# Kernel optimization log

Measured on AMD Instinct MI355X. Metric: run time of the kernel, lower is better.

Reference implementation:

```python
import jax, jax.numpy as jnp
import numpy as np

B, S, H = 2, 1024, 768
D, HID = 24, 96            # hdim_proj_dim, hdim_mlp_hidden
OUT_HID = 2 * max(128, H // 2)  # val_mlp hidden = 768
VAL_IN = 3 * H             # concat_hadam


def setup_inputs() -> dict:
    key = jax.random.key(0)
    ks = jax.random.split(key, 12)
    def w(k, shape, scale=0.02):
        return jax.random.normal(k, shape, dtype=jnp.float32) * scale
    return {
        "H_j": jax.random.normal(ks[0], (B, S, H), dtype=jnp.float32),
        "H_i": jax.random.normal(ks[1], (B, S, H), dtype=jnp.float32),
        "attn_mask": jnp.ones((B, S), dtype=jnp.float32),
        # p_j / p_i: Linear(H, D, bias=False), torch weight layout [D, H]
        "W_pj": w(ks[2], (D, H)),
        "W_pi": w(ks[3], (D, H)),
        # score_mlp: Linear(4D, HID) -> ReLU -> Linear(HID, 1)
        "W_s1": w(ks[4], (HID, 4 * D)),
        "b_s1": jnp.zeros((HID,), dtype=jnp.float32),
        "W_s2": w(ks[5], (1, HID)),
        "b_s2": jnp.zeros((1,), dtype=jnp.float32),
        # val_mlp: Linear(3H, OUT_HID) -> ReLU -> Linear(OUT_HID, H)
        "W_v1": w(ks[6], (OUT_HID, VAL_IN)),
        "b_v1": jnp.zeros((OUT_HID,), dtype=jnp.float32),
        "W_v2": w(ks[7], (H, OUT_HID)),
        "b_v2": jnp.zeros((H,), dtype=jnp.float32),
        "alpha": jnp.float32(0.05),  # init_gate_hdim
    }


def reference(H_j, H_i, attn_mask, W_pj, W_pi, W_s1, b_s1, W_s2, b_s2,
              W_v1, b_v1, W_v2, b_v2, alpha):
    # low-dim projections: [B,S,D]
    Zj = jnp.einsum('bsh,dh->bsd', H_j, W_pj)
    Zi = jnp.einsum('bsh,dh->bsd', H_i, W_pi)
    b, s, d = Zj.shape
    Zj_p = jnp.broadcast_to(Zj[:, :, None, :], (b, s, s, d))  # row = j (query)
    Zi_p = jnp.broadcast_to(Zi[:, None, :, :], (b, s, s, d))  # col = i (key)
    # 4-term pair features: [B,S,S,4D]
    pair = jnp.concatenate([Zj_p, Zi_p, Zj_p * Zi_p, jnp.abs(Zj_p - Zi_p)], axis=-1)
    # per-pair MLP -> scalar logit
    h = jax.nn.relu(jnp.einsum('bjif,hf->bjih', pair, W_s1) + b_s1)
    logits = jnp.einsum('bjih,oh->bjio', h, W_s2)[..., 0] + b_s2[0]  # [B,S,S]
    # additive key mask (mask over last dim = H_i positions)
    neg = jnp.finfo(logits.dtype).min
    logits = logits + (1.0 - attn_mask[:, None, :]) * neg
    # token_temp == 1.0 -> no temperature scaling
    probs = jax.nn.softmax(logits, axis=-1)
    ctx = jnp.einsum('bji,bih->bjh', probs, H_i)  # [B,S,H]
    # concat_hadam value features
    msg_in = jnp.concatenate([ctx, H_j, ctx * H_j], axis=-1)  # [B,S,3H]
    msg = jax.nn.relu(jnp.einsum('bsf,of->bso', msg_in, W_v1) + b_v1)
    msg = jnp.einsum('bso,ho->bsh', msg, W_v2) + b_v2
    # dropout is identity at inference; hdim_val_residual=False
    return alpha * msg
```

## Files before the change

### kernel.cpp

```cpp
#include <hip/hip_runtime.h>
#include <hip/hip_bf16.h>
#include <math.h>

#define B_ 2
#define S_ 1024
#define H_ 768
#define D_ 24
#define HID_ 96
#define OH_ 768
#define VI_ 2304

typedef short bf16x8 __attribute__((ext_vector_type(8)));
typedef float f32x4 __attribute__((ext_vector_type(4)));
typedef unsigned short u16;

static __device__ __forceinline__ float relu_(float x) { return x > 0.f ? x : 0.f; }

static __device__ __forceinline__ short f2bf(float f) {
    __hip_bfloat16 h = __float2bfloat16(f);
    return *reinterpret_cast<short*>(&h);
}
static __device__ __forceinline__ float bf2f(short s) {
    unsigned u = ((unsigned)(u16)s) << 16;
    return __uint_as_float(u);
}

static __device__ __forceinline__ void gl_lds16(const void* g, void* l) {
    __builtin_amdgcn_global_load_lds(
        (const __attribute__((address_space(1))) unsigned int*)g,
        (__attribute__((address_space(3))) unsigned int*)l, 16, 0, 0);
}

#define NEGF (-3.402823466e38f)

__global__ __launch_bounds__(256) void proj_kernel(
    const float* __restrict__ Hj, const float* __restrict__ Hi,
    const float* __restrict__ Wpj, const float* __restrict__ Wpi,
    float* __restrict__ Zj, float* __restrict__ Zi)
{
    __shared__ float rowj[H_], rowi[H_];
    const int t = blockIdx.x;
    const int tid = threadIdx.x;
    const float* hj = Hj + (size_t)t * H_;
    const float* hi = Hi + (size_t)t * H_;
    for (int x = tid; x < H_; x += 256) { rowj[x] = hj[x]; rowi[x] = hi[x]; }
    __syncthreads();

    const int g = tid & 7;
    for (int o = tid >> 3; o < 2 * D_; o += 32) {
        const float* row;
        const float* w;
        if (o < D_) { row = rowj; w = Wpj + o * H_; }
        else        { row = rowi; w = Wpi + (o - D_) * H_; }
        float s = 0.f;
        #pragma unroll 8
        for (int c = 0; c < H_ / 8; ++c) s += row[g + 8 * c] * w[g + 8 * c];
        s += __shfl_down(s, 4, 8);
        s += __shfl_down(s, 2, 8);
        s += __shfl_down(s, 1, 8);
        if (g == 0) {
            if (o < D_) Zj[(size_t)t * D_ + o] = s;
            else        Zi[(size_t)t * D_ + (o - D_)] = s;
        }
    }
}

__global__ __launch_bounds__(256) void pair_mfma_kernel(
    const float* __restrict__ Zj, const float* __restrict__ Zi,
    const float* __restrict__ Ws1, const float* __restrict__ Ws2,
    const float* __restrict__ bs1, const float* __restrict__ bs2,
    float* __restrict__ P)
{
    __shared__ float sZj32[16][28];
    __shared__ float sZi32[64][28];
    __shared__ short sZj16[16][24];
    __shared__ short sZi16[64][24];

    const int j0 = blockIdx.x * 16, i0 = blockIdx.y * 64, b = blockIdx.z;
    const int tid = threadIdx.x;
    const int lane = tid & 63, wv = tid >> 6;
    const int q = lane & 15, g = lane >> 4;

    for (int x = tid; x < 16 * D_; x += 256) {
        int r = x / D_, c = x % D_;
        float v = Zj[((size_t)(b * S_ + j0 + r)) * D_ + c];
        sZj32[r][c] = v; sZj16[r][c] = f2bf(v);
    }
    for (int x = tid; x < 64 * D_; x += 256) {
        int r = x / D_, c = x % D_;
        float v = Zi[((size_t)(b * S_ + i0 + r)) * D_ + c];
        sZi32[r][c] = v; sZi16[r][c] = f2bf(v);
    }

    bf16x8 wf[6][3];
    #pragma unroll
    for (int nt = 0; nt < 6; ++nt)
        #pragma unroll
        for (int ks = 0; ks < 3; ++ks) {
            const float* wp = Ws1 + (size_t)(nt * 16 + q) * 96 + ks * 32 + g * 8;
            bf16x8 t8;
            #pragma unroll
            for (int e = 0; e < 8; ++e) t8[e] = f2bf(wp[e]);
            wf[nt][ks] = t8;
        }
    float bias_r[6], w2_r[6];
    #pragma unroll
    for (int nt = 0; nt < 6; ++nt) {
        bias_r[nt] = bs1[nt * 16 + q];
        w2_r[nt]   = Ws2[nt * 16 + q];
    }
    const float b2 = bs2[0];
    __syncthreads();

    for (int m = 0; m < 16; ++m) {
        const int t = wv * 16 + m;
        const int jj = t >> 2, iibase = (t & 3) * 16;
        const int ii = iibase + q;

        bf16x8 af[3];
        #pragma unroll
        for (int ks = 0; ks < 3; ++ks) {
            const int c = ks * 4 + g;
            bf16x8 t8;
            if (c < 3) {
                t8 = *(const bf16x8*)&sZj16[jj][c * 8];
            } else if (c < 6) {
                t8 = *(const bf16x8*)&sZi16[ii][(c - 3) * 8];
            } else if (c < 9) {
                const float* zja = &sZj32[jj][(c - 6) * 8];
                const float* zia = &sZi32[ii][(c - 6) * 8];
                #pragma unroll
                for (int e = 0; e < 8; ++e) t8[e] = f2bf(zja[e] * zia[e]);
            } else {
                const float* zja = &sZj32[jj][(c - 9) * 8];
                const float* zia = &sZi32[ii][(c - 9) * 8];
                #pragma unroll
                for (int e = 0; e < 8; ++e) t8[e] = f2bf(fabsf(zja[e] - zia[e]));
            }
            af[ks] = t8;
        }

        f32x4 acc[6];
        #pragma unroll
        for (int nt = 0; nt < 6; ++nt) {
            f32x4 a = {0.f, 0.f, 0.f, 0.f};
            a = __builtin_amdgcn_mfma_f32_16x16x32_bf16(af[0], wf[nt][0], a, 0, 0, 0);
            a = __builtin_amdgcn_mfma_f32_16x16x32_bf16(af[1], wf[nt][1], a, 0, 0, 0);
            a = __builtin_amdgcn_mfma_f32_16x16x32_bf16(af[2], wf[nt][2], a, 0, 0, 0);
            acc[nt] = a;
        }

        float lg[4] = {0.f, 0.f, 0.f, 0.f};
        #pragma unroll
        for (int nt = 0; nt < 6; ++nt)
            #pragma unroll
            for (int r = 0; r < 4; ++r)
                lg[r] += w2_r[nt] * relu_(acc[nt][r] + bias_r[nt]);
        #pragma unroll
        for (int msk = 8; msk >= 1; msk >>= 1)
            #pragma unroll
            for (int r = 0; r < 4; ++r) lg[r] += __shfl_xor(lg[r], msk);

        if (q == 0) {
            float4 o = make_float4(lg[0] + b2, lg[1] + b2, lg[2] + b2, lg[3] + b2);
            *(float4*)&P[((size_t)(b * S_ + j0 + jj)) * S_ + i0 + iibase + g * 4] = o;
        }
    }
}

__global__ __launch_bounds__(256) void softmax_kernel(
    const float* __restrict__ mask, const float* __restrict__ P,
    u16* __restrict__ Pb)
{
    const int r = blockIdx.x;
    const int b = r / S_;
    const int tid = threadIdx.x;
    const float* row = P + (size_t)r * S_;
    __shared__ float red[4];

    float v[4];
    float mx = -INFINITY;
    #pragma unroll
    for (int c = 0; c < 4; ++c) {
        int i = tid + 256 * c;
        float m = mask[b * S_ + i];
        v[c] = row[i] + (1.0f - m) * NEGF;
        mx = fmaxf(mx, v[c]);
    }
    for (int off = 32; off > 0; off >>= 1) mx = fmaxf(mx, __shfl_xor(mx, off));
    if ((tid & 63) == 0) red[tid >> 6] = mx;
    __syncthreads();
    mx = fmaxf(fmaxf(red[0], red[1]), fmaxf(red[2], red[3]));

    float s = 0.f;
    #pragma unroll
    for (int c = 0; c < 4; ++c) { v[c] = __expf(v[c] - mx); s += v[c]; }
    for (int off = 32; off > 0; off >>= 1) s += __shfl_xor(s, off);
    __syncthreads();
    if ((tid & 63) == 0) red[tid >> 6] = s;
    __syncthreads();
    s = red[0] + red[1] + red[2] + red[3];
    const float inv = 1.0f / s;
    #pragma unroll
    for (int c = 0; c < 4; ++c)
        Pb[(size_t)r * S_ + tid + 256 * c] = (u16)f2bf(v[c] * inv);
}

__global__ __launch_bounds__(256) void cvt_kernel(
    const float* __restrict__ src, u16* __restrict__ dst, int n4)
{
    int i = blockIdx.x * 256 + threadIdx.x;
    if (i >= n4) return;
    float4 v = ((const float4*)src)[i];
    ushort4 o;
    o.x = (u16)f2bf(v.x); o.y = (u16)f2bf(v.y);
    o.z = (u16)f2bf(v.z); o.w = (u16)f2bf(v.w);
    ((ushort4*)dst)[i] = o;
}

__global__ __launch_bounds__(256) void transpose_hi_kernel(
    const float* __restrict__ Hi, u16* __restrict__ HiT)
{
    __shared__ u16 t[32][33];
    const int i0 = blockIdx.x * 32, h0 = blockIdx.y * 32, b = blockIdx.z;
    const int c = threadIdx.x & 31, r = threadIdx.x >> 5;
    #pragma unroll
    for (int rr = r; rr < 32; rr += 8)
        t[rr][c] = (u16)f2bf(Hi[((size_t)(b * S_ + i0 + rr)) * H_ + h0 + c]);
    __syncthreads();
    #pragma unroll
    for (int rr = r; rr < 32; rr += 8)
        HiT[((size_t)(b * H_ + h0 + rr)) * S_ + i0 + c] = t[c][rr];
}

__global__ __launch_bounds__(256) void msgin_kernel(
    const u16* __restrict__ ctx, const float* __restrict__ Hj,
    u16* __restrict__ MSG)
{
    const int idx = blockIdx.x * 256 + threadIdx.x;
    const int m = idx / 96, c8 = (idx % 96) * 8;
    bf16x8 c = *(const bf16x8*)&ctx[(size_t)m * H_ + c8];
    float4 h0 = *(const float4*)&Hj[(size_t)m * H_ + c8];
    float4 h1 = *(const float4*)&Hj[(size_t)m * H_ + c8 + 4];
    float hf[8] = {h0.x, h0.y, h0.z, h0.w, h1.x, h1.y, h1.z, h1.w};
    bf16x8 hb, pb;
    #pragma unroll
    for (int e = 0; e < 8; ++e) {
        hb[e] = f2bf(hf[e]);
        pb[e] = f2bf(bf2f(c[e]) * hf[e]);
    }
    u16* row = MSG + (size_t)m * VI_;
    *(bf16x8*)&row[c8]        = c;
    *(bf16x8*)&row[768 + c8]  = hb;
    *(bf16x8*)&row[1536 + c8] = pb;
}

template<int MODE, int K>
__global__ __launch_bounds__(256) void mfma_gemm_kernel(
    const u16* __restrict__ Ag, const u16* __restrict__ Bg,
    const float* __restrict__ bias, const float* __restrict__ alphaPtr,
    void* __restrict__ Outv)
{
    __shared__ u16 As[2][64 * 64];
    __shared__ u16 Bs[2][64 * 64];
    const int tid = threadIdx.x;
    const int lane = tid & 63, wv = tid >> 6;
    const int q = lane & 15, g = lane >> 4;
    const int wr = wv >> 1, wc = wv & 1;
    const int m0 = blockIdx.x * 64, n0 = blockIdx.y * 64;

    const u16* Ab = Ag + (size_t)m0 * K;
    const u16* Bb = (MODE == 0)
        ? Bg + (size_t)(m0 >> 10) * H_ * S_ + (size_t)n0 * K
        : Bg + (size_t)n0 * K;

    int st_r[2], st_gc[2], st_dst[2];
    #pragma unroll
    for (int it = 0; it < 2; ++it) {
        int cidx = (it * 4 + wv) * 64 + lane;
        st_r[it] = cidx >> 3;
        st_gc[it] = (cidx & 7) ^ (st_r[it] & 7);
        st_dst[it] = cidx * 8;
    }

    f32x4 acc[2][2] = {};

    auto stage = [&](int buf, int k0) {
        #pragma unroll
        for (int it = 0; it < 2; ++it) {
            gl_lds16(Ab + (size_t)st_r[it] * K + k0 + st_gc[it] * 8,
                     &As[buf][st_dst[it]]);
            gl_lds16(Bb + (size_t)st_r[it] * K + k0 + st_gc[it] * 8,
                     &Bs[buf][st_dst[it]]);
        }
    };
    auto comp = [&](int buf) {
        #pragma unroll
        for (int ks = 0; ks < 2; ++ks) {
            bf16x8 af[2], bfr[2];
            #pragma unroll
            for (int m = 0; m < 2; ++m) {
                int r = wr * 32 + m * 16 + q;
                int cl = (g + ks * 4) ^ (r & 7);
                af[m] = *(const bf16x8*)&As[buf][r * 64 + cl * 8];
            }
            #pragma unroll
            for (int n = 0; n < 2; ++n) {
                int r = wc * 32 + n * 16 + q;
                int cl = (g + ks * 4) ^ (r & 7);
                bfr[n] = *(const bf16x8*)&Bs[buf][r * 64 + cl * 8];
            }
            #pragma unroll
            for (int m = 0; m < 2; ++m)
                #pragma unroll
                for (int n = 0; n < 2; ++n)
                    acc[m][n] = __builtin_amdgcn_mfma_f32_16x16x32_bf16(
                        af[m], bfr[n], acc[m][n], 0, 0, 0);
        }
    };

    constexpr int NT = K / 64;
    stage(0, 0);
    __syncthreads();
    int cur = 0;
    for (int kt = 0; kt < NT - 1; ++kt) {
        stage(cur ^ 1, (kt + 1) * 64);
        comp(cur);
        __syncthreads();
        cur ^= 1;
    }
    comp(cur);

    const float alpha = (MODE == 2) ? alphaPtr[0] : 0.f;
    u16* O16 = (u16*)Outv;
    float* Of = (float*)Outv;
    #pragma unroll
    for (int m = 0; m < 2; ++m) {
        #pragma unroll
        for (int n = 0; n < 2; ++n) {
            const int col = n0 + wc * 32 + n * 16 + q;
            const float bn = (MODE == 0) ? 0.f : bias[col];
            #pragma unroll
            for (int rg = 0; rg < 4; ++rg) {
                const int row = m0 + wr * 32 + m * 16 + g * 4 + rg;
                float v = acc[m][n][rg];
                if (MODE == 0)      O16[(size_t)row * H_ + col] = (u16)f2bf(v);
                else if (MODE == 1) O16[(size_t)row * H_ + col] = (u16)f2bf(relu_(v + bn));
                else                Of[(size_t)row * H_ + col] = alpha * (v + bn);
            }
        }
    }
}

extern "C" void kernel_launch(void* const* d_in, const int* in_sizes, int n_in,
                              void* d_out, int out_size, void* d_ws, size_t ws_size,
                              hipStream_t stream)
{
    (void)in_sizes; (void)n_in; (void)out_size; (void)ws_size;
    const float* Hj   = (const float*)d_in[0];
    const float* Hi   = (const float*)d_in[1];
    const float* mask = (const float*)d_in[2];
    const float* Wpj  = (const float*)d_in[3];
    const float* Wpi  = (const float*)d_in[4];
    const float* Ws1  = (const float*)d_in[5];
    const float* bs1  = (const float*)d_in[6];
    const float* Ws2  = (const float*)d_in[7];
    const float* bs2  = (const float*)d_in[8];
    const float* Wv1  = (const float*)d_in[9];
    const float* bv1  = (const float*)d_in[10];
    const float* Wv2  = (const float*)d_in[11];
    const float* bv2  = (const float*)d_in[12];
    const float* alphaPtr = (const float*)d_in[13];
    float* out = (float*)d_out;

    char* w = (char*)d_ws;
    float* Zj   = (float*)(w);
    float* Zi   = (float*)(w + 196608);
    float* Plog = (float*)(w + 393216);
    u16*   Pb   = (u16*)  (w + 8782080 - 256);
    size_t oPlog = 393216;
    size_t oPb   = oPlog + 8388608;
    size_t oHiT  = oPb + 4194304;
    size_t oWv1b = oHiT + 3145728;
    size_t oWv2b = oWv1b + 3538944;
    size_t oCTX  = oWv2b + 1179648;
    Plog = (float*)(w + oPlog);
    Pb   = (u16*)(w + oPb);
    u16* HiT  = (u16*)(w + oHiT);
    u16* Wv1b = (u16*)(w + oWv1b);
    u16* Wv2b = (u16*)(w + oWv2b);
    u16* CTX  = (u16*)(w + oCTX);
    u16* MSG  = (u16*)(w + oPlog);
    u16* X1   = (u16*)(w + oHiT);

    cvt_kernel<<<(H_ * VI_ / 4 + 255) / 256, 256, 0, stream>>>(Wv1, Wv1b, H_ * VI_ / 4);
    cvt_kernel<<<(H_ * OH_ / 4 + 255) / 256, 256, 0, stream>>>(Wv2, Wv2b, H_ * OH_ / 4);
    transpose_hi_kernel<<<dim3(S_ / 32, H_ / 32, B_), 256, 0, stream>>>(Hi, HiT);

    proj_kernel<<<B_ * S_, 256, 0, stream>>>(Hj, Hi, Wpj, Wpi, Zj, Zi);
    pair_mfma_kernel<<<dim3(S_ / 16, S_ / 64, B_), 256, 0, stream>>>(
        Zj, Zi, Ws1, Ws2, bs1, bs2, Plog);
    softmax_kernel<<<B_ * S_, 256, 0, stream>>>(mask, Plog, Pb);

    mfma_gemm_kernel<0, S_><<<dim3(2048 / 64, H_ / 64), 256, 0, stream>>>(
        Pb, HiT, nullptr, nullptr, CTX);
    msgin_kernel<<<(2048 * 96) / 256, 256, 0, stream>>>(CTX, Hj, MSG);
    mfma_gemm_kernel<1, VI_><<<dim3(2048 / 64, OH_ / 64), 256, 0, stream>>>(
        MSG, Wv1b, bv1, nullptr, X1);
    mfma_gemm_kernel<2, OH_><<<dim3(2048 / 64, H_ / 64), 256, 0, stream>>>(
        X1, Wv2b, bv2, alphaPtr, out);
}
```

Baseline: 265.5 us.

## Precompute per-query Zj term of score MLP and shrink pair MFMA K

The first score-MLP layer is split so that the Zj-only contribution (W_s1[:, :D]·Zj + b_s1) is computed once per query row in fp32 and used as the MFMA accumulator initial value. The per-pair MFMA then only covers the Zi, product and abs-diff blocks, each padded to K=32. The MFMA output layout is swapped so that hidden units sit along rows, and LDS tiles get XOR swizzling to avoid bank conflicts. The aim is to cut redundant Zj work and conversions inside the pair kernel's hot loop, at the cost of extra LDS, a small precompute stage and zero-padded K lanes.

```diff
diff --git a/kernel.cpp b/kernel.cpp
--- a/kernel.cpp
+++ b/kernel.cpp
@@ -71,99 +71,117 @@
     const float* __restrict__ bs1, const float* __restrict__ bs2,
     float* __restrict__ P)
 {
-    __shared__ float sZj32[16][28];
-    __shared__ float sZi32[64][28];
-    __shared__ short sZj16[16][24];
-    __shared__ short sZi16[64][24];
+    __shared__ float sZj32[16 * 32];
+    __shared__ float sZi32[64 * 32];
+    __shared__ u16   sZi16[64 * 64];
+    __shared__ float sAterm[16 * 96];
+    __shared__ float sW1a[96 * 25];
+    __shared__ float sW2[96];
 
     const int j0 = blockIdx.x * 16, i0 = blockIdx.y * 64, b = blockIdx.z;
     const int tid = threadIdx.x;
     const int lane = tid & 63, wv = tid >> 6;
     const int q = lane & 15, g = lane >> 4;
 
-    for (int x = tid; x < 16 * D_; x += 256) {
-        int r = x / D_, c = x % D_;
-        float v = Zj[((size_t)(b * S_ + j0 + r)) * D_ + c];
-        sZj32[r][c] = v; sZj16[r][c] = f2bf(v);
-    }
-    for (int x = tid; x < 64 * D_; x += 256) {
-        int r = x / D_, c = x % D_;
-        float v = Zi[((size_t)(b * S_ + i0 + r)) * D_ + c];
-        sZi32[r][c] = v; sZi16[r][c] = f2bf(v);
-    }
-
-    bf16x8 wf[6][3];
-    #pragma unroll
-    for (int nt = 0; nt < 6; ++nt)
-        #pragma unroll
-        for (int ks = 0; ks < 3; ++ks) {
-            const float* wp = Ws1 + (size_t)(nt * 16 + q) * 96 + ks * 32 + g * 8;
-            bf16x8 t8;
-            #pragma unroll
-            for (int e = 0; e < 8; ++e) t8[e] = f2bf(wp[e]);
-            wf[nt][ks] = t8;
-        }
-    float bias_r[6], w2_r[6];
-    #pragma unroll
-    for (int nt = 0; nt < 6; ++nt) {
-        bias_r[nt] = bs1[nt * 16 + q];
-        w2_r[nt]   = Ws2[nt * 16 + q];
-    }
+    if (tid < 128) {
+        int r = tid >> 3, d = tid & 7;
+        float4 v = make_float4(0.f, 0.f, 0.f, 0.f);
+        if (d < 6) v = *(const float4*)&Zj[((size_t)(b * S_ + j0 + r)) * D_ + 4 * d];
+        *(float4*)&sZj32[r * 32 + 4 * d] = v;
+    }
+    for (int t = tid; t < 512; t += 256) {
+        int r = t >> 3, d = t & 7;
+        int gr = d ^ (r & 7);
+        float4 v = make_float4(0.f, 0.f, 0.f, 0.f);
+        if (d < 6) v = *(const float4*)&Zi[((size_t)(b * S_ + i0 + r)) * D_ + 4 * d];
+        *(float4*)&sZi32[r * 32 + 4 * gr] = v;
+    }
+    {
+        int r = tid >> 2, c = tid & 3;
+        int gr = c ^ (r & 7);
+        bf16x8 o = {0, 0, 0, 0, 0, 0, 0, 0};
+        if (c < 3) {
+            const float* src = &Zi[((size_t)(b * S_ + i0 + r)) * D_ + 8 * c];
+            #pragma unroll
+            for (int e = 0; e < 8; ++e) o[e] = f2bf(src[e]);
+        }
+        *(bf16x8*)&sZi16[r * 64 + 8 * gr] = o;
+    }
+    for (int t = tid; t < 96 * 24; t += 256) {
+        int k = t / 24, d = t - k * 24;
+        sW1a[k * 25 + d] = Ws1[(size_t)k * 96 + d];
+    }
+    if (tid < 96) sW2[tid] = Ws2[tid];
+    __syncthreads();
+
+    for (int o = tid; o < 16 * 96; o += 256) {
+        int j = o / 96, k = o - j * 96;
+        float acc = bs1[k];
+        #pragma unroll
+        for (int d = 0; d < 24; ++d) acc += sW1a[k * 25 + d] * sZj32[j * 32 + d];
+        sAterm[o] = acc;
+    }
+
+    bf16x8 wf[3][6];
+    #pragma unroll
+    for (int s = 0; s < 3; ++s)
+        #pragma unroll
+        for (int nt = 0; nt < 6; ++nt) {
+            bf16x8 t8 = {0, 0, 0, 0, 0, 0, 0, 0};
+            if (g < 3) {
+                const float* wp = Ws1 + (size_t)(nt * 16 + q) * 96 + 24 * (s + 1) + 8 * g;
+                #pragma unroll
+                for (int e = 0; e < 8; ++e) t8[e] = f2bf(wp[e]);
+            }
+            wf[s][nt] = t8;
+        }
     const float b2 = bs2[0];
     __syncthreads();
 
-    for (int m = 0; m < 16; ++m) {
-        const int t = wv * 16 + m;
-        const int jj = t >> 2, iibase = (t & 3) * 16;
-        const int ii = iibase + q;
-
-        bf16x8 af[3];
-        #pragma unroll
-        for (int ks = 0; ks < 3; ++ks) {
-            const int c = ks * 4 + g;
-            bf16x8 t8;
-            if (c < 3) {
-                t8 = *(const bf16x8*)&sZj16[jj][c * 8];
-            } else if (c < 6) {
-                t8 = *(const bf16x8*)&sZi16[ii][(c - 3) * 8];
-            } else if (c < 9) {
-                const float* zja = &sZj32[jj][(c - 6) * 8];
-                const float* zia = &sZi32[ii][(c - 6) * 8];
+    for (int jq = 0; jq < 4; ++jq) {
+        const int jj = wv * 4 + jq;
+        const f32x4 zjA = *(const f32x4*)&sZj32[jj * 32 + 8 * g];
+        const f32x4 zjB = *(const f32x4*)&sZj32[jj * 32 + 8 * g + 4];
+        f32x4 At[6];
+        #pragma unroll
+        for (int nt = 0; nt < 6; ++nt)
+            At[nt] = *(const f32x4*)&sAterm[jj * 96 + nt * 16 + 4 * g];
+
+        #pragma unroll
+        for (int ib = 0; ib < 4; ++ib) {
+            const int ii = ib * 16 + q;
+            const int sw = ii & 7;
+            bf16x8 af1 = *(const bf16x8*)&sZi16[ii * 64 + 8 * (g ^ sw)];
+            f32x4 zi0 = *(const f32x4*)&sZi32[ii * 32 + 4 * ((2 * g) ^ sw)];
+            f32x4 zi1 = *(const f32x4*)&sZi32[ii * 32 + 4 * ((2 * g + 1) ^ sw)];
+            bf16x8 af2, af3;
+            #pragma unroll
+            for (int e = 0; e < 4; ++e) {
+                af2[e]     = f2bf(zjA[e] * zi0[e]);
+                af2[e + 4] = f2bf(zjB[e] * zi1[e]);
+                af3[e]     = f2bf(fabsf(zjA[e] - zi0[e]));
+                af3[e + 4] = f2bf(fabsf(zjB[e] - zi1[e]));
+            }
+            f32x4 acc[6];
+            #pragma unroll
+            for (int nt = 0; nt < 6; ++nt) acc[nt] = At[nt];
+            #pragma unroll
+            for (int nt = 0; nt < 6; ++nt) {
+                acc[nt] = __builtin_amdgcn_mfma_f32_16x16x32_bf16(wf[0][nt], af1, acc[nt], 0, 0, 0);
+                acc[nt] = __builtin_amdgcn_mfma_f32_16x16x32_bf16(wf[1][nt], af2, acc[nt], 0, 0, 0);
+                acc[nt] = __builtin_amdgcn_mfma_f32_16x16x32_bf16(wf[2][nt], af3, acc[nt], 0, 0, 0);
+            }
+            float lg = 0.f;
+            #pragma unroll
+            for (int nt = 0; nt < 6; ++nt) {
+                f32x4 w2v = *(const f32x4*)&sW2[nt * 16 + 4 * g];
                 #pragma unroll
-                for (int e = 0; e < 8; ++e) t8[e] = f2bf(zja[e] * zia[e]);
-            } else {
-                const float* zja = &sZj32[jj][(c - 9) * 8];
-                const float* zia = &sZi32[ii][(c - 9) * 8];
-                #pragma unroll
-                for (int e = 0; e < 8; ++e) t8[e] = f2bf(fabsf(zja[e] - zia[e]));
-            }
-            af[ks] = t8;
-        }
-
-        f32x4 acc[6];
-        #pragma unroll
-        for (int nt = 0; nt < 6; ++nt) {
-            f32x4 a = {0.f, 0.f, 0.f, 0.f};
-            a = __builtin_amdgcn_mfma_f32_16x16x32_bf16(af[0], wf[nt][0], a, 0, 0, 0);
-            a = __builtin_amdgcn_mfma_f32_16x16x32_bf16(af[1], wf[nt][1], a, 0, 0, 0);
-            a = __builtin_amdgcn_mfma_f32_16x16x32_bf16(af[2], wf[nt][2], a, 0, 0, 0);
-            acc[nt] = a;
-        }
-
-        float lg[4] = {0.f, 0.f, 0.f, 0.f};
-        #pragma unroll
-        for (int nt = 0; nt < 6; ++nt)
-            #pragma unroll
-            for (int r = 0; r < 4; ++r)
-                lg[r] += w2_r[nt] * relu_(acc[nt][r] + bias_r[nt]);
-        #pragma unroll
-        for (int msk = 8; msk >= 1; msk >>= 1)
-            #pragma unroll
-            for (int r = 0; r < 4; ++r) lg[r] += __shfl_xor(lg[r], msk);
-
-        if (q == 0) {
-            float4 o = make_float4(lg[0] + b2, lg[1] + b2, lg[2] + b2, lg[3] + b2);
-            *(float4*)&P[((size_t)(b * S_ + j0 + jj)) * S_ + i0 + iibase + g * 4] = o;
+                for (int r = 0; r < 4; ++r) lg += w2v[r] * relu_(acc[nt][r]);
+            }
+            lg += __shfl_xor(lg, 16);
+            lg += __shfl_xor(lg, 32);
+            if (lane < 16)
+                P[((size_t)(b * S_ + j0 + jj)) * S_ + i0 + ib * 16 + lane] = lg + b2;
         }
     }
 }
@@ -376,16 +394,14 @@
     char* w = (char*)d_ws;
     float* Zj   = (float*)(w);
     float* Zi   = (float*)(w + 196608);
-    float* Plog = (float*)(w + 393216);
-    u16*   Pb   = (u16*)  (w + 8782080 - 256);
     size_t oPlog = 393216;
     size_t oPb   = oPlog + 8388608;
     size_t oHiT  = oPb + 4194304;
     size_t oWv1b = oHiT + 3145728;
     size_t oWv2b = oWv1b + 3538944;
     size_t oCTX  = oWv2b + 1179648;
-    Plog = (float*)(w + oPlog);
-    Pb   = (u16*)(w + oPb);
+    float* Plog = (float*)(w + oPlog);
+    u16* Pb   = (u16*)(w + oPb);
     u16* HiT  = (u16*)(w + oHiT);
     u16* Wv1b = (u16*)(w + oWv1b);
     u16* Wv2b = (u16*)(w + oWv2b);
```

Result: faster. 256.5 us (-3.4%).
